# Kernel optimization log

Hardware: AMD Instinct MI355X
Metric: run time of the kernel (lower is better)

## Reference

```python
import jax, jax.numpy as jnp
import numpy as np

N = 200000      # nodes per graph batch side
E = 3200000     # edges per side (avg degree 16)
NG = 1000       # number of graphs per side
CIN = 64
F1, F2, F3, D = 64, 32, 16, 16
BN_EPS = 1e-5


def gin_conv(x, edge_index, eps, W1, b1, W2, b2, gamma, beta):
    # GINConv: nn((1+eps)*x + sum_{j->i} x_j), nn = Lin-ReLU-Lin-BatchNorm1d (batch stats)
    src, dst = edge_index[0], edge_index[1]
    agg = jax.ops.segment_sum(x[src], dst, num_segments=x.shape[0])
    h = (1.0 + eps) * x + agg
    h = jax.nn.relu(h @ W1 + b1) @ W2 + b2
    mu = jnp.mean(h, axis=0)
    var = jnp.var(h, axis=0)
    return gamma * (h - mu) * jax.lax.rsqrt(var + BN_EPS) + beta


def global_attention_readout(x, batch, W, b):
    # global_mean_pool -> sigmoid fc -> gated global_add_pool
    ones = jnp.ones((x.shape[0], 1), x.dtype)
    cnt = jax.ops.segment_sum(ones, batch, num_segments=NG)
    summ = jax.ops.segment_sum(x, batch, num_segments=NG)
    mean = summ / jnp.maximum(cnt, 1.0)
    c = jax.nn.sigmoid(mean @ W + b)          # [NG, F3]
    c_n = c[batch]                             # broadcast back to nodes
    gate = jax.nn.sigmoid(jnp.sum(x * c_n, axis=1, keepdims=True))
    return jax.ops.segment_sum(gate * x, batch, num_segments=NG)


def efn(h_i, h_j, aW1, ab1, aW2, ab2, mW, mb):
    h = jnp.concatenate([h_i, h_j], axis=1)   # [NG, 2*F3]
    att = jnp.tanh(jax.nn.relu(h @ aW1 + ab1) @ aW2 + ab2)
    enc = att * h + h
    return jax.nn.relu(enc @ mW + mb)         # [NG, D]


def setup_inputs() -> dict:
    key = jax.random.key(0)
    ks = iter(jax.random.split(key, 48))
    def nrm(shape, s=0.1):
        return jax.random.normal(next(ks), shape, jnp.float32) * s
    inp = {}
    inp["x_i"] = jax.random.normal(next(ks), (N, CIN), jnp.float32)
    inp["x_j"] = jax.random.normal(next(ks), (N, CIN), jnp.float32)
    inp["edge_index_i"] = jax.random.randint(next(ks), (2, E), 0, N, dtype=jnp.int32)
    inp["edge_index_j"] = jax.random.randint(next(ks), (2, E), 0, N, dtype=jnp.int32)
    inp["batch_i"] = jnp.sort(jax.random.randint(next(ks), (N,), 0, NG, dtype=jnp.int32))
    inp["batch_j"] = jnp.sort(jax.random.randint(next(ks), (N,), 0, NG, dtype=jnp.int32))
    # GINConv 1 (train_eps=True, init 0)
    inp["eps1"] = jnp.zeros((), jnp.float32)
    inp["g1_W1"], inp["g1_b1"] = nrm((CIN, F1)), jnp.zeros((F1,), jnp.float32)
    inp["g1_W2"], inp["g1_b2"] = nrm((F1, F1)), jnp.zeros((F1,), jnp.float32)
    inp["g1_g"], inp["g1_bt"] = jnp.ones((F1,), jnp.float32), jnp.zeros((F1,), jnp.float32)
    inp["eps2"] = jnp.zeros((), jnp.float32)
    inp["g2_W1"], inp["g2_b1"] = nrm((F1, F2)), jnp.zeros((F2,), jnp.float32)
    inp["g2_W2"], inp["g2_b2"] = nrm((F2, F2)), jnp.zeros((F2,), jnp.float32)
    inp["g2_g"], inp["g2_bt"] = jnp.ones((F2,), jnp.float32), jnp.zeros((F2,), jnp.float32)
    inp["eps3"] = jnp.zeros((), jnp.float32)
    inp["g3_W1"], inp["g3_b1"] = nrm((F2, F3)), jnp.zeros((F3,), jnp.float32)
    inp["g3_W2"], inp["g3_b2"] = nrm((F3, F3)), jnp.zeros((F3,), jnp.float32)
    inp["g3_g"], inp["g3_bt"] = jnp.ones((F3,), jnp.float32), jnp.zeros((F3,), jnp.float32)
    # global attention fc
    inp["att_W"], inp["att_b"] = nrm((F3, F3)), jnp.zeros((F3,), jnp.float32)
    # EFN: in=2*F3=32, reduction=4 -> 8
    inp["efn_aW1"], inp["efn_ab1"] = nrm((2 * F3, 8)), jnp.zeros((8,), jnp.float32)
    inp["efn_aW2"], inp["efn_ab2"] = nrm((8, 2 * F3)), jnp.zeros((2 * F3,), jnp.float32)
    inp["efn_mW"], inp["efn_mb"] = nrm((2 * F3, D)), jnp.zeros((D,), jnp.float32)
    # final fc: D -> D//2 -> 1
    inp["fc_W1"], inp["fc_b1"] = nrm((D, D // 2)), jnp.zeros((D // 2,), jnp.float32)
    inp["fc_W2"], inp["fc_b2"] = nrm((D // 2, 1)), jnp.zeros((1,), jnp.float32)
    return inp


def reference(x_i, x_j, edge_index_i, edge_index_j, batch_i, batch_j,
              eps1, g1_W1, g1_b1, g1_W2, g1_b2, g1_g, g1_bt,
              eps2, g2_W1, g2_b1, g2_W2, g2_b2, g2_g, g2_bt,
              eps3, g3_W1, g3_b1, g3_W2, g3_b2, g3_g, g3_bt,
              att_W, att_b,
              efn_aW1, efn_ab1, efn_aW2, efn_ab2, efn_mW, efn_mb,
              fc_W1, fc_b1, fc_W2, fc_b2):
    xi1 = gin_conv(x_i, edge_index_i, eps1, g1_W1, g1_b1, g1_W2, g1_b2, g1_g, g1_bt)
    xj1 = gin_conv(x_j, edge_index_j, eps1, g1_W1, g1_b1, g1_W2, g1_b2, g1_g, g1_bt)
    xi2 = gin_conv(xi1, edge_index_i, eps2, g2_W1, g2_b1, g2_W2, g2_b2, g2_g, g2_bt)
    xj2 = gin_conv(xj1, edge_index_j, eps2, g2_W1, g2_b1, g2_W2, g2_b2, g2_g, g2_bt)
    xi3 = gin_conv(xi2, edge_index_i, eps3, g3_W1, g3_b1, g3_W2, g3_b2, g3_g, g3_bt)
    xj3 = gin_conv(xj2, edge_index_j, eps3, g3_W1, g3_b1, g3_W2, g3_b2, g3_g, g3_bt)
    h_i = global_attention_readout(xi3, batch_i, att_W, att_b)
    h_j = global_attention_readout(xj3, batch_j, att_W, att_b)
    h_AB = efn(h_i, h_j, efn_aW1, efn_ab1, efn_aW2, efn_ab2, efn_mW, efn_mb)
    h_AA = efn(h_i, h_i, efn_aW1, efn_ab1, efn_aW2, efn_ab2, efn_mW, efn_mb)
    h_BB = efn(h_j, h_j, efn_aW1, efn_ab1, efn_aW2, efn_ab2, efn_mW, efn_mb)
    h_Ab = h_AB - h_BB
    h_aB = h_AB - h_AA
    score = (jax.nn.relu(h_AB @ fc_W1 + fc_b1) @ fc_W2 + fc_b2).squeeze(1)
    return (score, h_Ab, h_aB)
```

## Files before the change

kernel.cpp:

```cpp
#include <hip/hip_runtime.h>
#include <math.h>

#define NGRAPH 1000
#define NBK_MAX 400
#define PART_BLOCKS 256

typedef unsigned short ushort_t;
typedef __attribute__((ext_vector_type(8))) short short8;
typedef __attribute__((ext_vector_type(4))) float floatx4;

static __device__ inline ushort_t f2bf(float f) {
  unsigned u = __float_as_uint(f);
  u = (u + 0x7fffu + ((u >> 16) & 1u)) >> 16;
  return (ushort_t)u;
}


__global__ __launch_bounds__(1024) void bucket_hist(const int* __restrict__ dst, int E, int chunk,
                                                    int* __restrict__ hist, int nbk) {
  __shared__ int lh[NBK_MAX];
  for (int i = threadIdx.x; i < nbk; i += 1024) lh[i] = 0;
  __syncthreads();
  const int e0 = blockIdx.x * chunk;
  const int e1 = min(E, e0 + chunk);
  for (int e = e0 + threadIdx.x; e < e1; e += 1024) atomicAdd(&lh[dst[e] >> 9], 1);
  __syncthreads();
  int* row = hist + (size_t)blockIdx.x * nbk;
  for (int i = threadIdx.x; i < nbk; i += 1024) row[i] = lh[i];
}

__global__ __launch_bounds__(PART_BLOCKS) void colscan_par(int* __restrict__ hist, int nbk,
                                                           int* __restrict__ totals) {
  __shared__ int s[PART_BLOCKS];
  const int b = blockIdx.x;
  const int t = threadIdx.x;
  s[t] = hist[(size_t)t * nbk + b];
  __syncthreads();
  for (int off = 1; off < PART_BLOCKS; off <<= 1) {
    int u = (t >= off) ? s[t - off] : 0;
    __syncthreads();
    s[t] += u;
    __syncthreads();
  }
  const int exc = (t == 0) ? 0 : s[t - 1];
  hist[(size_t)t * nbk + b] = exc;
  if (t == PART_BLOCKS - 1) totals[b] = s[PART_BLOCKS - 1];
}

__global__ __launch_bounds__(1024) void scan_small(const int* __restrict__ in, int n,
                                                   int* __restrict__ out) {
  __shared__ int s[2048];
  const int t = threadIdx.x;
  s[t] = (t < n) ? in[t] : 0;
  s[t + 1024] = (t + 1024 < n) ? in[t + 1024] : 0;
  __syncthreads();
  for (int off = 1; off < 2048; off <<= 1) {
    int v0 = (t >= off) ? s[t - off] : 0;
    int v1 = ((t + 1024) >= off) ? s[t + 1024 - off] : 0;
    __syncthreads();
    s[t] += v0;
    s[t + 1024] += v1;
    __syncthreads();
  }
  if (t < n) out[t] = (t == 0) ? 0 : s[t - 1];
  const int u = t + 1024;
  if (u < n) out[u] = s[u - 1];
  if (t == 0) out[n] = s[n - 1];
}

__global__ __launch_bounds__(1024) void partition_kernel(const int* __restrict__ src,
                                                         const int* __restrict__ dst, int E,
                                                         int chunk, const int* __restrict__ hist,
                                                         const int* __restrict__ boff,
                                                         unsigned* __restrict__ ebuf, int nbk) {
  __shared__ int lbase[NBK_MAX];
  __shared__ int lcur[NBK_MAX];
  const int* row = hist + (size_t)blockIdx.x * nbk;
  for (int i = threadIdx.x; i < nbk; i += 1024) {
    lbase[i] = boff[i] + row[i];
    lcur[i] = 0;
  }
  __syncthreads();
  const int e0 = blockIdx.x * chunk;
  const int e1 = min(E, e0 + chunk);
  for (int e = e0 + threadIdx.x; e < e1; e += 1024) {
    int d = dst[e];
    int b = d >> 9;
    int pos = lbase[b] + atomicAdd(&lcur[b], 1);
    ebuf[pos] = ((unsigned)src[e] << 9) | (unsigned)(d & 511);
  }
}

__global__ __launch_bounds__(512) void bucket_csr(const unsigned* __restrict__ ebuf,
                                                  const int* __restrict__ boff,
                                                  int* __restrict__ row_ptr, int* __restrict__ col,
                                                  int N, int E) {
  __shared__ int cnt[512], cur[512];
  const int b = blockIdx.x;
  const int node0 = b << 9;
  const int nn = min(512, N - node0);
  const int es = boff[b], ee = boff[b + 1];
  const int t = threadIdx.x;
  cnt[t] = 0;
  __syncthreads();
  for (int e = es + t; e < ee; e += 512) atomicAdd(&cnt[ebuf[e] & 511u], 1);
  __syncthreads();
  for (int off = 1; off < 512; off <<= 1) {
    int v = (t >= off) ? cnt[t - off] : 0;
    __syncthreads();
    cnt[t] += v;
    __syncthreads();
  }
  int ex = (t == 0) ? 0 : cnt[t - 1];
  cur[t] = ex;
  if (t < nn) row_ptr[node0 + t] = es + ex;
  __syncthreads();
  for (int e = es + t; e < ee; e += 512) {
    unsigned u = ebuf[e];
    int li = (int)(u & 511u);
    int pos = es + atomicAdd(&cur[li], 1);
    col[pos] = (int)(u >> 9);
  }
  if (b == 0 && t == 0) row_ptr[N] = E;
}


template <int FIN, int FOUT, bool HAS_BN>
__global__ __launch_bounds__(256) void lin_mfma(const float* __restrict__ x,
                                                const float* __restrict__ W,
                                                const float* __restrict__ stats,
                                                const float* __restrict__ gamma,
                                                const float* __restrict__ beta, float invN,
                                                ushort_t* __restrict__ y, int n) {
  constexpr int KC = FIN / 32;
  constexpr int FT = FOUT / 16;
  __shared__ ushort_t Wbf[FIN * FOUT];
  __shared__ float scv[FIN], ofv[FIN];
  const int tid = threadIdx.x;
  for (int i = tid; i < FIN * FOUT; i += 256) Wbf[i] = f2bf(W[i]);
  for (int i = tid; i < FIN; i += 256) {
    if (HAS_BN) {
      float mu = stats[i] * invN;
      float var = stats[128 + i] * invN - mu * mu;
      float s = gamma[i] * rsqrtf(var + 1e-5f);
      scv[i] = s;
      ofv[i] = beta[i] - s * mu;
    } else {
      scv[i] = 1.f;
      ofv[i] = 0.f;
    }
  }
  __syncthreads();
  const int lane = tid & 63, wv = tid >> 6;
  const int colf = lane & 15, quad = lane >> 4, kbase = quad * 8;

  short8 Bf[FT][KC];
#pragma unroll
  for (int t = 0; t < FT; t++)
#pragma unroll
    for (int c = 0; c < KC; c++)
#pragma unroll
      for (int j = 0; j < 8; j++)
        Bf[t][c][j] = (short)Wbf[(c * 32 + kbase + j) * FOUT + t * 16 + colf];

  const floatx4 zero4 = {0.f, 0.f, 0.f, 0.f};
  const int ntiles = (n + 15) >> 4;
  for (int nt = blockIdx.x * 4 + wv; nt < ntiles; nt += gridDim.x * 4) {
    const int node0 = nt << 4;
    const int anode = node0 + colf;
    short8 Af[KC];
#pragma unroll
    for (int c = 0; c < KC; c++) {
      if (anode < n) {
        const int kk = c * 32 + kbase;
        const float* xp = x + (size_t)anode * FIN + kk;
        float4 xa = *(const float4*)xp;
        float4 xb = *(const float4*)(xp + 4);
        Af[c][0] = (short)f2bf(fmaf(xa.x, scv[kk + 0], ofv[kk + 0]));
        Af[c][1] = (short)f2bf(fmaf(xa.y, scv[kk + 1], ofv[kk + 1]));
        Af[c][2] = (short)f2bf(fmaf(xa.z, scv[kk + 2], ofv[kk + 2]));
        Af[c][3] = (short)f2bf(fmaf(xa.w, scv[kk + 3], ofv[kk + 3]));
        Af[c][4] = (short)f2bf(fmaf(xb.x, scv[kk + 4], ofv[kk + 4]));
        Af[c][5] = (short)f2bf(fmaf(xb.y, scv[kk + 5], ofv[kk + 5]));
        Af[c][6] = (short)f2bf(fmaf(xb.z, scv[kk + 6], ofv[kk + 6]));
        Af[c][7] = (short)f2bf(fmaf(xb.w, scv[kk + 7], ofv[kk + 7]));
      } else {
        Af[c] = short8{0, 0, 0, 0, 0, 0, 0, 0};
      }
    }
#pragma unroll
    for (int t = 0; t < FT; t++) {
      floatx4 acc = zero4;
#pragma unroll
      for (int c = 0; c < KC; c++)
        acc = __builtin_amdgcn_mfma_f32_16x16x32_bf16(Af[c], Bf[t][c], acc, 0, 0, 0);
#pragma unroll
      for (int r = 0; r < 4; r++) {
        const int row = node0 + quad * 4 + r;
        if (row < n) y[(size_t)row * FOUT + t * 16 + colf] = f2bf(acc[r]);
      }
    }
  }
}


template <int F>
__global__ __launch_bounds__(256) void lin2s_mfma(const ushort_t* __restrict__ m,
                                                  const float* __restrict__ W,
                                                  const float* __restrict__ b,
                                                  float* __restrict__ h,
                                                  float* __restrict__ stats, int n) {
  constexpr int KC = (F + 31) / 32;
  constexpr int FT = F / 16;
  __shared__ ushort_t Wbf[F * F];
  __shared__ float bs[F], ls[F], lsq[F];
  const int tid = threadIdx.x;
  for (int i = tid; i < F * F; i += 256) Wbf[i] = f2bf(W[i]);
  if (tid < F) {
    bs[tid] = b[tid];
    ls[tid] = 0.f;
    lsq[tid] = 0.f;
  }
  __syncthreads();
  const int lane = tid & 63, wv = tid >> 6;
  const int colf = lane & 15, quad = lane >> 4, kbase = quad * 8;

  short8 Bf[FT][KC];
#pragma unroll
  for (int t = 0; t < FT; t++)
#pragma unroll
    for (int c = 0; c < KC; c++)
#pragma unroll
      for (int j = 0; j < 8; j++) {
        const int k = c * 32 + kbase + j;
        Bf[t][c][j] = (k < F) ? (short)Wbf[k * F + t * 16 + colf] : (short)0;
      }

  const floatx4 zero4 = {0.f, 0.f, 0.f, 0.f};
  float ssum[FT], ssq[FT];
#pragma unroll
  for (int t = 0; t < FT; t++) {
    ssum[t] = 0.f;
    ssq[t] = 0.f;
  }

  const int ntiles = (n + 15) >> 4;
  for (int nt = blockIdx.x * 4 + wv; nt < ntiles; nt += gridDim.x * 4) {
    const int node0 = nt << 4;
    const int anode = node0 + colf;
    short8 Af[KC];
#pragma unroll
    for (int c = 0; c < KC; c++) {
      const int kk = c * 32 + kbase;
      if (anode < n && kk < F)
        Af[c] = *(const short8*)(m + (size_t)anode * F + kk);
      else
        Af[c] = short8{0, 0, 0, 0, 0, 0, 0, 0};
    }
#pragma unroll
    for (int t = 0; t < FT; t++) {
      floatx4 acc = zero4;
#pragma unroll
      for (int c = 0; c < KC; c++)
        acc = __builtin_amdgcn_mfma_f32_16x16x32_bf16(Af[c], Bf[t][c], acc, 0, 0, 0);
      const float bv = bs[t * 16 + colf];
#pragma unroll
      for (int r = 0; r < 4; r++) {
        const int row = node0 + quad * 4 + r;
        if (row < n) {
          float o = acc[r] + bv;
          h[(size_t)row * F + t * 16 + colf] = o;
          ssum[t] += o;
          ssq[t] += o * o;
        }
      }
    }
  }
#pragma unroll
  for (int t = 0; t < FT; t++) {
    atomicAdd(&ls[t * 16 + colf], ssum[t]);
    atomicAdd(&lsq[t * 16 + colf], ssq[t]);
  }
  __syncthreads();
  if (tid < F) {
    atomicAdd(&stats[tid], ls[tid]);
    atomicAdd(&stats[128 + tid], lsq[tid]);
  }
}


template <int F>
__global__ __launch_bounds__(256) void aggrelu_b(const ushort_t* __restrict__ y,
                                                 const int* __restrict__ row_ptr,
                                                 const int* __restrict__ col,
                                                 const float* __restrict__ epsp,
                                                 const float* __restrict__ b1,
                                                 ushort_t* __restrict__ m, int n) {
  constexpr int LPN = F / 8;
  constexpr int NPB = 256 / LPN;
  const int tid = threadIdx.x;
  const int ln = tid / LPN;
  const int fl = tid % LPN;
  const float e1 = 1.0f + epsp[0];
  const float4 b1a = ((const float4*)b1)[fl * 2];
  const float4 b1b = ((const float4*)b1)[fl * 2 + 1];

  const int node = blockIdx.x * NPB + ln;
  if (node >= n) return;
  const uint4* yr = (const uint4*)y;
  const size_t rowi = (size_t)node * LPN + fl;
  const int rs = row_ptr[node], re = row_ptr[node + 1];

  float acc[8];
#pragma unroll
  for (int j = 0; j < 8; j++) acc[j] = 0.f;

  auto addv = [&](uint4 v) {
    acc[0] += __uint_as_float(v.x << 16);
    acc[1] += __uint_as_float(v.x & 0xffff0000u);
    acc[2] += __uint_as_float(v.y << 16);
    acc[3] += __uint_as_float(v.y & 0xffff0000u);
    acc[4] += __uint_as_float(v.z << 16);
    acc[5] += __uint_as_float(v.z & 0xffff0000u);
    acc[6] += __uint_as_float(v.w << 16);
    acc[7] += __uint_as_float(v.w & 0xffff0000u);
  };

  int e = rs;
  for (; e + 8 <= re; e += 8) {
    int c0 = col[e], c1 = col[e + 1], c2 = col[e + 2], c3 = col[e + 3];
    int c4 = col[e + 4], c5 = col[e + 5], c6 = col[e + 6], c7 = col[e + 7];
    uint4 v0 = yr[(size_t)c0 * LPN + fl];
    uint4 v1 = yr[(size_t)c1 * LPN + fl];
    uint4 v2 = yr[(size_t)c2 * LPN + fl];
    uint4 v3 = yr[(size_t)c3 * LPN + fl];
    uint4 v4 = yr[(size_t)c4 * LPN + fl];
    uint4 v5 = yr[(size_t)c5 * LPN + fl];
    uint4 v6 = yr[(size_t)c6 * LPN + fl];
    uint4 v7 = yr[(size_t)c7 * LPN + fl];
    addv(v0);
    addv(v1);
    addv(v2);
    addv(v3);
    addv(v4);
    addv(v5);
    addv(v6);
    addv(v7);
  }
  for (; e + 4 <= re; e += 4) {
    int c0 = col[e], c1 = col[e + 1], c2 = col[e + 2], c3 = col[e + 3];
    uint4 v0 = yr[(size_t)c0 * LPN + fl];
    uint4 v1 = yr[(size_t)c1 * LPN + fl];
    uint4 v2 = yr[(size_t)c2 * LPN + fl];
    uint4 v3 = yr[(size_t)c3 * LPN + fl];
    addv(v0);
    addv(v1);
    addv(v2);
    addv(v3);
  }
  for (; e < re; e++) addv(yr[(size_t)col[e] * LPN + fl]);

  uint4 sv = yr[rowi];
  float r0, r1, r2, r3, r4, r5, r6, r7;
  r0 = fmaxf(fmaf(e1, __uint_as_float(sv.x << 16), acc[0]) + b1a.x, 0.f);
  r1 = fmaxf(fmaf(e1, __uint_as_float(sv.x & 0xffff0000u), acc[1]) + b1a.y, 0.f);
  r2 = fmaxf(fmaf(e1, __uint_as_float(sv.y << 16), acc[2]) + b1a.z, 0.f);
  r3 = fmaxf(fmaf(e1, __uint_as_float(sv.y & 0xffff0000u), acc[3]) + b1a.w, 0.f);
  r4 = fmaxf(fmaf(e1, __uint_as_float(sv.z << 16), acc[4]) + b1b.x, 0.f);
  r5 = fmaxf(fmaf(e1, __uint_as_float(sv.z & 0xffff0000u), acc[5]) + b1b.y, 0.f);
  r6 = fmaxf(fmaf(e1, __uint_as_float(sv.w << 16), acc[6]) + b1b.z, 0.f);
  r7 = fmaxf(fmaf(e1, __uint_as_float(sv.w & 0xffff0000u), acc[7]) + b1b.w, 0.f);
  uint4 o;
  o.x = (unsigned)f2bf(r0) | ((unsigned)f2bf(r1) << 16);
  o.y = (unsigned)f2bf(r2) | ((unsigned)f2bf(r3) << 16);
  o.z = (unsigned)f2bf(r4) | ((unsigned)f2bf(r5) << 16);
  o.w = (unsigned)f2bf(r6) | ((unsigned)f2bf(r7) << 16);
  ((uint4*)m)[rowi] = o;
}


__global__ __launch_bounds__(256) void readout_fused(
    const float* __restrict__ h3, const int* __restrict__ batch, int n,
    const float* __restrict__ stats, const float* __restrict__ gamma,
    const float* __restrict__ beta, float invN, const float* __restrict__ attW,
    const float* __restrict__ attb, float* __restrict__ hg, int ng) {
  __shared__ float sM[16], oM[16], red[16][17], meanM[16], cM[16];
  __shared__ int seg[2];
  const int tid = threadIdx.x;
  const int g = blockIdx.x;
  const int f = tid & 15, slot = tid >> 4;
  if (tid < 16) {
    float mu = stats[tid] * invN;
    float var = stats[128 + tid] * invN - mu * mu;
    float s = gamma[tid] * rsqrtf(var + 1e-5f);
    sM[tid] = s;
    oM[tid] = beta[tid] - s * mu;
  }
  if (tid >= 32 && tid < 34) {
    const int key = g + (tid - 32);
    int lo = 0, hi = n;
    while (lo < hi) {
      int mid = (lo + hi) >> 1;
      if (batch[mid] < key) lo = mid + 1; else hi = mid;
    }
    seg[tid - 32] = lo;
  }
  __syncthreads();
  const int s0 = seg[0], e0 = seg[1];
  const float sf = sM[f], of = oM[f];

  float acc = 0.f;
  for (int node = s0 + slot; node < e0; node += 16)
    acc += fmaf(h3[(size_t)node * 16 + f], sf, of);
  red[slot][f] = acc;
  __syncthreads();
  if (tid < 16) {
    float t = 0.f;
    for (int s = 0; s < 16; s++) t += red[s][tid];
    meanM[tid] = t / fmaxf((float)(e0 - s0), 1.f);
  }
  __syncthreads();
  if (tid < 16) {
    float a = attb[tid];
    for (int k = 0; k < 16; k++) a += meanM[k] * attW[k * 16 + tid];
    cM[tid] = 1.f / (1.f + expf(-a));
  }
  __syncthreads();
  const float cf = cM[f];
  float acc2 = 0.f;
  for (int node = s0 + slot; node < e0; node += 16) {
    float xv = fmaf(h3[(size_t)node * 16 + f], sf, of);
    float p = xv * cf;
    for (int m = 8; m >= 1; m >>= 1) p += __shfl_xor(p, m, 16);
    acc2 += xv / (1.f + expf(-p));
  }
  red[slot][f] = acc2;
  __syncthreads();
  if (tid < 16) {
    float t = 0.f;
    for (int s = 0; s < 16; s++) t += red[s][tid];
    hg[g * 16 + tid] = t;
  }
}


__global__ __launch_bounds__(256) void final3_kernel(
    const float* __restrict__ hgA, const float* __restrict__ hgB, const float* __restrict__ aW1,
    const float* __restrict__ ab1, const float* __restrict__ aW2, const float* __restrict__ ab2,
    const float* __restrict__ mW, const float* __restrict__ mb, const float* __restrict__ fcW1,
    const float* __restrict__ fcb1, const float* __restrict__ fcW2,
    const float* __restrict__ fcb2, float* __restrict__ out, int ng) {
  __shared__ float aW1s[256], aW2s[256], mWs[512], fcW1s[128];
  __shared__ float ab1s[8], ab2s[32], mbs[16], fcb1s[8], fcW2s[8];
  __shared__ float fcb2s;
  __shared__ float hb[16][33], m8b[16][9], encb[16][33], abb[16][17], tb[16][9];
  const int tid = threadIdx.x;
  aW1s[tid] = aW1[tid];
  aW2s[tid] = aW2[tid];
  mWs[tid] = mW[tid];
  mWs[256 + tid] = mW[256 + tid];
  if (tid < 128) fcW1s[tid] = fcW1[tid];
  if (tid < 8) {
    ab1s[tid] = ab1[tid];
    fcb1s[tid] = fcb1[tid];
    fcW2s[tid] = fcW2[tid];
  }
  if (tid < 32) ab2s[tid] = ab2[tid];
  if (tid < 16) mbs[tid] = mb[tid];
  if (tid == 0) fcb2s = fcb2[0];
  __syncthreads();

  const int g = tid >> 4;
  const int l = tid & 15;
  const int gg = blockIdx.x * 16 + g;
  const bool valid = gg < ng;
  const float hiv = valid ? hgA[gg * 16 + l] : 0.f;
  const float hjv = valid ? hgB[gg * 16 + l] : 0.f;
  float res[3];

#pragma unroll
  for (int p = 0; p < 3; p++) {
    float ha = (p == 2) ? hjv : hiv;
    float h2 = (p == 1) ? hiv : hjv;
    hb[g][l] = ha;
    hb[g][16 + l] = h2;
    __syncthreads();
    if (l < 8) {
      float t = ab1s[l];
#pragma unroll
      for (int k = 0; k < 32; k++) t += hb[g][k] * aW1s[k * 8 + l];
      m8b[g][l] = fmaxf(t, 0.f);
    }
    __syncthreads();
    float e0 = ab2s[l], e1 = ab2s[16 + l];
#pragma unroll
    for (int k = 0; k < 8; k++) {
      float mv = m8b[g][k];
      e0 += mv * aW2s[k * 32 + l];
      e1 += mv * aW2s[k * 32 + 16 + l];
    }
    float a0 = tanhf(e0), a1 = tanhf(e1);
    encb[g][l] = fmaf(a0, ha, ha);
    encb[g][16 + l] = fmaf(a1, h2, h2);
    __syncthreads();
    float o = mbs[l];
#pragma unroll
    for (int k = 0; k < 32; k++) o += encb[g][k] * mWs[k * 16 + l];
    res[p] = fmaxf(o, 0.f);
    __syncthreads();
  }

  if (valid) {
    out[ng + gg * 16 + l] = res[0] - res[2];
    out[ng + ng * 16 + gg * 16 + l] = res[0] - res[1];
  }
  abb[g][l] = res[0];
  __syncthreads();
  if (l < 8) {
    float t = fcb1s[l];
#pragma unroll
    for (int k = 0; k < 16; k++) t += abb[g][k] * fcW1s[k * 8 + l];
    tb[g][l] = fmaxf(t, 0.f);
  }
  __syncthreads();
  if (l == 0 && valid) {
    float sc = fcb2s;
#pragma unroll
    for (int o = 0; o < 8; o++) sc += tb[g][o] * fcW2s[o];
    out[gg] = sc;
  }
}


extern "C" void kernel_launch(void* const* d_in, const int* in_sizes, int n_in, void* d_out,
                              int out_size, void* d_ws, size_t ws_size, hipStream_t stream) {
  (void)n_in;
  (void)out_size;
  (void)ws_size;
  const int N = in_sizes[0] / 64;
  const int E = in_sizes[2] / 2;
  const int NG = NGRAPH;
  const int NBK = (N + 511) >> 9;
  const int CHUNK = (E + PART_BLOCKS - 1) / PART_BLOCKS;

  char* w = (char*)d_ws;
  auto alloc = [&](size_t bytes) -> void* {
    void* p = (void*)w;
    w += (bytes + 255) & ~(size_t)255;
    return p;
  };
  int* row_ptr = (int*)alloc((size_t)(N + 1) * 4);
  int* col = (int*)alloc((size_t)E * 4);
  int* hist = (int*)alloc((size_t)PART_BLOCKS * NBK * 4);
  int* totals = (int*)alloc((size_t)NBK * 4);
  int* boff = (int*)alloc((size_t)(NBK + 1) * 4);
  float* bufA = (float*)alloc((size_t)N * 64 * 4);
  float* bufB = (float*)alloc((size_t)N * 64 * 4);
  float* stats = (float*)alloc(3 * 256 * 4);
  float* hgA = (float*)alloc((size_t)NG * 16 * 4);
  float* hgB = (float*)alloc((size_t)NG * 16 * 4);

  unsigned* ebuf = (unsigned*)bufA;
  ushort_t* y1 = (ushort_t*)bufB;
  ushort_t* m1 = (ushort_t*)bufA;
  float* h1 = bufB;
  ushort_t* y2 = (ushort_t*)bufA;
  ushort_t* m2 = (ushort_t*)(bufA + (size_t)N * 16);
  float* h2 = bufB;
  ushort_t* y3 = (ushort_t*)bufA;
  ushort_t* m3 = (ushort_t*)(bufA + (size_t)N * 8);
  float* h3 = bufB;

  const float* attW = (const float*)d_in[27];
  const float* attb = (const float*)d_in[28];
  const float invN = 1.0f / (float)N;

  for (int s = 0; s < 2; s++) {
    const float* x0 = (const float*)d_in[s];
    const int* esrc = (const int*)d_in[2 + s];
    const int* edst = esrc + E;
    const int* batch = (const int*)d_in[4 + s];
    float* hg = s ? hgB : hgA;

    bucket_hist<<<PART_BLOCKS, 1024, 0, stream>>>(edst, E, CHUNK, hist, NBK);
    colscan_par<<<NBK, PART_BLOCKS, 0, stream>>>(hist, NBK, totals);
    scan_small<<<1, 1024, 0, stream>>>(totals, NBK, boff);
    partition_kernel<<<PART_BLOCKS, 1024, 0, stream>>>(esrc, edst, E, CHUNK, hist, boff, ebuf,
                                                       NBK);
    bucket_csr<<<NBK, 512, 0, stream>>>(ebuf, boff, row_ptr, col, N, E);

    hipMemsetAsync(stats, 0, 3 * 256 * 4, stream);

    lin_mfma<64, 64, false><<<512, 256, 0, stream>>>(
        x0, (const float*)d_in[7], nullptr, nullptr, nullptr, invN, y1, N);
    aggrelu_b<64><<<(N + 31) / 32, 256, 0, stream>>>(
        y1, row_ptr, col, (const float*)d_in[6], (const float*)d_in[8], m1, N);
    lin2s_mfma<64><<<512, 256, 0, stream>>>(m1, (const float*)d_in[9], (const float*)d_in[10],
                                            h1, stats, N);

    lin_mfma<64, 32, true><<<512, 256, 0, stream>>>(
        h1, (const float*)d_in[14], stats, (const float*)d_in[11], (const float*)d_in[12], invN,
        y2, N);
    aggrelu_b<32><<<(N + 63) / 64, 256, 0, stream>>>(
        y2, row_ptr, col, (const float*)d_in[13], (const float*)d_in[15], m2, N);
    lin2s_mfma<32><<<512, 256, 0, stream>>>(m2, (const float*)d_in[16], (const float*)d_in[17],
                                            h2, stats + 256, N);

    lin_mfma<32, 16, true><<<512, 256, 0, stream>>>(
        h2, (const float*)d_in[21], stats + 256, (const float*)d_in[18], (const float*)d_in[19],
        invN, y3, N);
    aggrelu_b<16><<<(N + 127) / 128, 256, 0, stream>>>(
        y3, row_ptr, col, (const float*)d_in[20], (const float*)d_in[22], m3, N);
    lin2s_mfma<16><<<512, 256, 0, stream>>>(m3, (const float*)d_in[23], (const float*)d_in[24],
                                            h3, stats + 512, N);

    readout_fused<<<NG, 256, 0, stream>>>(h3, batch, N, stats + 512, (const float*)d_in[25],
                                          (const float*)d_in[26], invN, attW, attb, hg, NG);
  }

  final3_kernel<<<(NG + 15) / 16, 256, 0, stream>>>(
      hgA, hgB, (const float*)d_in[29], (const float*)d_in[30], (const float*)d_in[31],
      (const float*)d_in[32], (const float*)d_in[33], (const float*)d_in[34],
      (const float*)d_in[35], (const float*)d_in[36], (const float*)d_in[37],
      (const float*)d_in[38], (float*)d_out, NG);
}
```

Baseline: 894.5 us.

## Store GIN hidden activations in fp16 and build both CSRs in batched launches

The lin2s outputs (h1, h2, h3) are now stored as fp16 instead of fp32, and the consuming lin_mfma and readout kernels read them as half. Those GEMMs also switch from bf16 to fp16 MFMA, with weights and inputs converted to _Float16. The bucket-sort CSR construction for both graph sides now runs as single 2D-grid launches instead of being repeated inside the per-side loop, so separate row_ptr/col buffers are kept per side. The aim is to halve activation memory traffic and give the CSR build kernels twice the blocks per launch. The cost is reduced precision and range on the intermediates, with a risk of fp16 overflow or accuracy loss.

```diff
diff --git a/kernel.cpp b/kernel.cpp
--- a/kernel.cpp
+++ b/kernel.cpp
@@ -7,6 +7,7 @@
 
 typedef unsigned short ushort_t;
 typedef __attribute__((ext_vector_type(8))) short short8;
+typedef __attribute__((ext_vector_type(8))) _Float16 half8;
 typedef __attribute__((ext_vector_type(4))) float floatx4;
 
 static __device__ inline ushort_t f2bf(float f) {
@@ -14,10 +15,19 @@
   u = (u + 0x7fffu + ((u >> 16) & 1u)) >> 16;
   return (ushort_t)u;
 }
-
-
-__global__ __launch_bounds__(1024) void bucket_hist(const int* __restrict__ dst, int E, int chunk,
-                                                    int* __restrict__ hist, int nbk) {
+static __device__ inline ushort_t f2h_bits(float f) {
+  return __builtin_bit_cast(ushort_t, (_Float16)f);
+}
+static __device__ inline float h2f_bits(ushort_t u) {
+  return (float)__builtin_bit_cast(_Float16, u);
+}
+
+
+__global__ __launch_bounds__(1024) void bucket_hist2(const int* __restrict__ dst0,
+                                                     const int* __restrict__ dst1, int E,
+                                                     int chunk, int* __restrict__ hist, int nbk) {
+  const int side = blockIdx.y;
+  const int* __restrict__ dst = side ? dst1 : dst0;
   __shared__ int lh[NBK_MAX];
   for (int i = threadIdx.x; i < nbk; i += 1024) lh[i] = 0;
   __syncthreads();
@@ -25,16 +35,19 @@
   const int e1 = min(E, e0 + chunk);
   for (int e = e0 + threadIdx.x; e < e1; e += 1024) atomicAdd(&lh[dst[e] >> 9], 1);
   __syncthreads();
-  int* row = hist + (size_t)blockIdx.x * nbk;
+  int* row = hist + ((size_t)side * PART_BLOCKS + blockIdx.x) * nbk;
   for (int i = threadIdx.x; i < nbk; i += 1024) row[i] = lh[i];
 }
 
-__global__ __launch_bounds__(PART_BLOCKS) void colscan_par(int* __restrict__ hist, int nbk,
-                                                           int* __restrict__ totals) {
+__global__ __launch_bounds__(PART_BLOCKS) void colscan_par2(int* __restrict__ hist, int nbk,
+                                                            int* __restrict__ totals) {
   __shared__ int s[PART_BLOCKS];
+  const int side = blockIdx.y;
+  int* __restrict__ hist_s = hist + (size_t)side * PART_BLOCKS * nbk;
+  int* __restrict__ totals_s = totals + side * nbk;
   const int b = blockIdx.x;
   const int t = threadIdx.x;
-  s[t] = hist[(size_t)t * nbk + b];
+  s[t] = hist_s[(size_t)t * nbk + b];
   __syncthreads();
   for (int off = 1; off < PART_BLOCKS; off <<= 1) {
     int u = (t >= off) ? s[t - off] : 0;
@@ -43,16 +56,19 @@
     __syncthreads();
   }
   const int exc = (t == 0) ? 0 : s[t - 1];
-  hist[(size_t)t * nbk + b] = exc;
-  if (t == PART_BLOCKS - 1) totals[b] = s[PART_BLOCKS - 1];
-}
-
-__global__ __launch_bounds__(1024) void scan_small(const int* __restrict__ in, int n,
-                                                   int* __restrict__ out) {
+  hist_s[(size_t)t * nbk + b] = exc;
+  if (t == PART_BLOCKS - 1) totals_s[b] = s[PART_BLOCKS - 1];
+}
+
+__global__ __launch_bounds__(1024) void scan_small2(const int* __restrict__ in, int n,
+                                                    int* __restrict__ out) {
   __shared__ int s[2048];
+  const int side = blockIdx.x;
+  const int* __restrict__ in_s = in + side * n;
+  int* __restrict__ out_s = out + side * (n + 1);
   const int t = threadIdx.x;
-  s[t] = (t < n) ? in[t] : 0;
-  s[t + 1024] = (t + 1024 < n) ? in[t + 1024] : 0;
+  s[t] = (t < n) ? in_s[t] : 0;
+  s[t + 1024] = (t + 1024 < n) ? in_s[t + 1024] : 0;
   __syncthreads();
   for (int off = 1; off < 2048; off <<= 1) {
     int v0 = (t >= off) ? s[t - off] : 0;
@@ -62,22 +78,30 @@
     s[t + 1024] += v1;
     __syncthreads();
   }
-  if (t < n) out[t] = (t == 0) ? 0 : s[t - 1];
+  if (t < n) out_s[t] = (t == 0) ? 0 : s[t - 1];
   const int u = t + 1024;
-  if (u < n) out[u] = s[u - 1];
-  if (t == 0) out[n] = s[n - 1];
-}
-
-__global__ __launch_bounds__(1024) void partition_kernel(const int* __restrict__ src,
-                                                         const int* __restrict__ dst, int E,
-                                                         int chunk, const int* __restrict__ hist,
-                                                         const int* __restrict__ boff,
-                                                         unsigned* __restrict__ ebuf, int nbk) {
+  if (u < n) out_s[u] = s[u - 1];
+  if (t == 0) out_s[n] = s[n - 1];
+}
+
+__global__ __launch_bounds__(1024) void partition2(const int* __restrict__ src0,
+                                                   const int* __restrict__ src1,
+                                                   const int* __restrict__ dst0,
+                                                   const int* __restrict__ dst1, int E, int chunk,
+                                                   const int* __restrict__ hist,
+                                                   const int* __restrict__ boff,
+                                                   unsigned* __restrict__ ebufA,
+                                                   unsigned* __restrict__ ebufB, int nbk) {
+  const int side = blockIdx.y;
+  const int* __restrict__ src = side ? src1 : src0;
+  const int* __restrict__ dst = side ? dst1 : dst0;
+  const int* __restrict__ boff_s = boff + side * (nbk + 1);
+  unsigned* __restrict__ ebuf = side ? ebufB : ebufA;
   __shared__ int lbase[NBK_MAX];
   __shared__ int lcur[NBK_MAX];
-  const int* row = hist + (size_t)blockIdx.x * nbk;
+  const int* row = hist + ((size_t)side * PART_BLOCKS + blockIdx.x) * nbk;
   for (int i = threadIdx.x; i < nbk; i += 1024) {
-    lbase[i] = boff[i] + row[i];
+    lbase[i] = boff_s[i] + row[i];
     lcur[i] = 0;
   }
   __syncthreads();
@@ -91,15 +115,24 @@
   }
 }
 
-__global__ __launch_bounds__(512) void bucket_csr(const unsigned* __restrict__ ebuf,
-                                                  const int* __restrict__ boff,
-                                                  int* __restrict__ row_ptr, int* __restrict__ col,
-                                                  int N, int E) {
+__global__ __launch_bounds__(512) void bucket_csr2(const unsigned* __restrict__ ebufA,
+                                                   const unsigned* __restrict__ ebufB,
+                                                   const int* __restrict__ boff,
+                                                   int* __restrict__ row_ptrA,
+                                                   int* __restrict__ colA,
+                                                   int* __restrict__ row_ptrB,
+                                                   int* __restrict__ colB, int N, int E,
+                                                   int nbk) {
   __shared__ int cnt[512], cur[512];
+  const int side = blockIdx.y;
+  const unsigned* __restrict__ ebuf = side ? ebufB : ebufA;
+  const int* __restrict__ boff_s = boff + side * (nbk + 1);
+  int* __restrict__ row_ptr = side ? row_ptrB : row_ptrA;
+  int* __restrict__ col = side ? colB : colA;
   const int b = blockIdx.x;
   const int node0 = b << 9;
   const int nn = min(512, N - node0);
-  const int es = boff[b], ee = boff[b + 1];
+  const int es = boff_s[b], ee = boff_s[b + 1];
   const int t = threadIdx.x;
   cnt[t] = 0;
   __syncthreads();
@@ -125,8 +158,8 @@
 }
 
 
-template <int FIN, int FOUT, bool HAS_BN>
-__global__ __launch_bounds__(256) void lin_mfma(const float* __restrict__ x,
+template <int FIN, int FOUT, bool HAS_BN, bool IN_HALF>
+__global__ __launch_bounds__(256) void lin_mfma(const void* __restrict__ xin,
                                                 const float* __restrict__ W,
                                                 const float* __restrict__ stats,
                                                 const float* __restrict__ gamma,
@@ -134,12 +167,12 @@
                                                 ushort_t* __restrict__ y, int n) {
   constexpr int KC = FIN / 32;
   constexpr int FT = FOUT / 16;
-  __shared__ ushort_t Wbf[FIN * FOUT];
+  __shared__ _Float16 Whf[FIN * FOUT];
   __shared__ float scv[FIN], ofv[FIN];
   const int tid = threadIdx.x;
-  for (int i = tid; i < FIN * FOUT; i += 256) Wbf[i] = f2bf(W[i]);
+  for (int i = tid; i < FIN * FOUT; i += 256) Whf[i] = (_Float16)W[i];
   for (int i = tid; i < FIN; i += 256) {
-    if (HAS_BN) {
+    if constexpr (HAS_BN) {
       float mu = stats[i] * invN;
       float var = stats[128 + i] * invN - mu * mu;
       float s = gamma[i] * rsqrtf(var + 1e-5f);
@@ -154,38 +187,46 @@
   const int lane = tid & 63, wv = tid >> 6;
   const int colf = lane & 15, quad = lane >> 4, kbase = quad * 8;
 
-  short8 Bf[FT][KC];
+  half8 Bf[FT][KC];
 #pragma unroll
   for (int t = 0; t < FT; t++)
 #pragma unroll
     for (int c = 0; c < KC; c++)
 #pragma unroll
       for (int j = 0; j < 8; j++)
-        Bf[t][c][j] = (short)Wbf[(c * 32 + kbase + j) * FOUT + t * 16 + colf];
+        Bf[t][c][j] = Whf[(c * 32 + kbase + j) * FOUT + t * 16 + colf];
 
   const floatx4 zero4 = {0.f, 0.f, 0.f, 0.f};
   const int ntiles = (n + 15) >> 4;
   for (int nt = blockIdx.x * 4 + wv; nt < ntiles; nt += gridDim.x * 4) {
     const int node0 = nt << 4;
     const int anode = node0 + colf;
-    short8 Af[KC];
+    half8 Af[KC];
 #pragma unroll
     for (int c = 0; c < KC; c++) {
       if (anode < n) {
         const int kk = c * 32 + kbase;
-        const float* xp = x + (size_t)anode * FIN + kk;
-        float4 xa = *(const float4*)xp;
-        float4 xb = *(const float4*)(xp + 4);
-        Af[c][0] = (short)f2bf(fmaf(xa.x, scv[kk + 0], ofv[kk + 0]));
-        Af[c][1] = (short)f2bf(fmaf(xa.y, scv[kk + 1], ofv[kk + 1]));
-        Af[c][2] = (short)f2bf(fmaf(xa.z, scv[kk + 2], ofv[kk + 2]));
-        Af[c][3] = (short)f2bf(fmaf(xa.w, scv[kk + 3], ofv[kk + 3]));
-        Af[c][4] = (short)f2bf(fmaf(xb.x, scv[kk + 4], ofv[kk + 4]));
-        Af[c][5] = (short)f2bf(fmaf(xb.y, scv[kk + 5], ofv[kk + 5]));
-        Af[c][6] = (short)f2bf(fmaf(xb.z, scv[kk + 6], ofv[kk + 6]));
-        Af[c][7] = (short)f2bf(fmaf(xb.w, scv[kk + 7], ofv[kk + 7]));
+        if constexpr (IN_HALF) {
+          const ushort_t* hp = (const ushort_t*)xin + (size_t)anode * FIN + kk;
+          half8 hv = *(const half8*)hp;
+#pragma unroll
+          for (int j = 0; j < 8; j++)
+            Af[c][j] = (_Float16)fmaf((float)hv[j], scv[kk + j], ofv[kk + j]);
+        } else {
+          const float* xp = (const float*)xin + (size_t)anode * FIN + kk;
+          float4 xa = *(const float4*)xp;
+          float4 xb = *(const float4*)(xp + 4);
+          Af[c][0] = (_Float16)fmaf(xa.x, scv[kk + 0], ofv[kk + 0]);
+          Af[c][1] = (_Float16)fmaf(xa.y, scv[kk + 1], ofv[kk + 1]);
+          Af[c][2] = (_Float16)fmaf(xa.z, scv[kk + 2], ofv[kk + 2]);
+          Af[c][3] = (_Float16)fmaf(xa.w, scv[kk + 3], ofv[kk + 3]);
+          Af[c][4] = (_Float16)fmaf(xb.x, scv[kk + 4], ofv[kk + 4]);
+          Af[c][5] = (_Float16)fmaf(xb.y, scv[kk + 5], ofv[kk + 5]);
+          Af[c][6] = (_Float16)fmaf(xb.z, scv[kk + 6], ofv[kk + 6]);
+          Af[c][7] = (_Float16)fmaf(xb.w, scv[kk + 7], ofv[kk + 7]);
+        }
       } else {
-        Af[c] = short8{0, 0, 0, 0, 0, 0, 0, 0};
+        Af[c] = half8{0, 0, 0, 0, 0, 0, 0, 0};
       }
     }
 #pragma unroll
@@ -193,7 +234,7 @@
       floatx4 acc = zero4;
 #pragma unroll
       for (int c = 0; c < KC; c++)
-        acc = __builtin_amdgcn_mfma_f32_16x16x32_bf16(Af[c], Bf[t][c], acc, 0, 0, 0);
+        acc = __builtin_amdgcn_mfma_f32_16x16x32_f16(Af[c], Bf[t][c], acc, 0, 0, 0);
 #pragma unroll
       for (int r = 0; r < 4; r++) {
         const int row = node0 + quad * 4 + r;
@@ -208,7 +249,7 @@
 __global__ __launch_bounds__(256) void lin2s_mfma(const ushort_t* __restrict__ m,
                                                   const float* __restrict__ W,
                                                   const float* __restrict__ b,
-                                                  float* __restrict__ h,
+                                                  ushort_t* __restrict__ h,
                                                   float* __restrict__ stats, int n) {
   constexpr int KC = (F + 31) / 32;
   constexpr int FT = F / 16;
@@ -269,7 +310,7 @@
         const int row = node0 + quad * 4 + r;
         if (row < n) {
           float o = acc[r] + bv;
-          h[(size_t)row * F + t * 16 + colf] = o;
+          h[(size_t)row * F + t * 16 + colf] = f2h_bits(o);
           ssum[t] += o;
           ssq[t] += o * o;
         }
@@ -380,7 +421,7 @@
 
 
 __global__ __launch_bounds__(256) void readout_fused(
-    const float* __restrict__ h3, const int* __restrict__ batch, int n,
+    const ushort_t* __restrict__ h3, const int* __restrict__ batch, int n,
     const float* __restrict__ stats, const float* __restrict__ gamma,
     const float* __restrict__ beta, float invN, const float* __restrict__ attW,
     const float* __restrict__ attb, float* __restrict__ hg, int ng) {
@@ -411,7 +452,7 @@
 
   float acc = 0.f;
   for (int node = s0 + slot; node < e0; node += 16)
-    acc += fmaf(h3[(size_t)node * 16 + f], sf, of);
+    acc += fmaf(h2f_bits(h3[(size_t)node * 16 + f]), sf, of);
   red[slot][f] = acc;
   __syncthreads();
   if (tid < 16) {
@@ -429,7 +470,7 @@
   const float cf = cM[f];
   float acc2 = 0.f;
   for (int node = s0 + slot; node < e0; node += 16) {
-    float xv = fmaf(h3[(size_t)node * 16 + f], sf, of);
+    float xv = fmaf(h2f_bits(h3[(size_t)node * 16 + f]), sf, of);
     float p = xv * cf;
     for (int m = 8; m >= 1; m >>= 1) p += __shfl_xor(p, m, 16);
     acc2 += xv / (1.f + expf(-p));
@@ -549,72 +590,80 @@
     w += (bytes + 255) & ~(size_t)255;
     return p;
   };
-  int* row_ptr = (int*)alloc((size_t)(N + 1) * 4);
-  int* col = (int*)alloc((size_t)E * 4);
-  int* hist = (int*)alloc((size_t)PART_BLOCKS * NBK * 4);
-  int* totals = (int*)alloc((size_t)NBK * 4);
-  int* boff = (int*)alloc((size_t)(NBK + 1) * 4);
-  float* bufA = (float*)alloc((size_t)N * 64 * 4);
-  float* bufB = (float*)alloc((size_t)N * 64 * 4);
-  float* stats = (float*)alloc(3 * 256 * 4);
+  int* row_ptrA = (int*)alloc((size_t)(N + 1) * 4);
+  int* colA = (int*)alloc((size_t)E * 4);
+  int* row_ptrB = (int*)alloc((size_t)(N + 1) * 4);
+  int* colB = (int*)alloc((size_t)E * 4);
+  int* hist = (int*)alloc((size_t)2 * PART_BLOCKS * NBK * 4);
+  int* totals = (int*)alloc((size_t)2 * NBK * 4);
+  int* boff = (int*)alloc((size_t)2 * (NBK + 1) * 4);
+  ushort_t* bufA = (ushort_t*)alloc((size_t)N * 64 * 2);
+  ushort_t* bufB = (ushort_t*)alloc((size_t)N * 64 * 2);
+  float* stats = (float*)alloc((size_t)2 * 768 * 4);
   float* hgA = (float*)alloc((size_t)NG * 16 * 4);
   float* hgB = (float*)alloc((size_t)NG * 16 * 4);
 
-  unsigned* ebuf = (unsigned*)bufA;
-  ushort_t* y1 = (ushort_t*)bufB;
-  ushort_t* m1 = (ushort_t*)bufA;
-  float* h1 = bufB;
-  ushort_t* y2 = (ushort_t*)bufA;
-  ushort_t* m2 = (ushort_t*)(bufA + (size_t)N * 16);
-  float* h2 = bufB;
-  ushort_t* y3 = (ushort_t*)bufA;
-  ushort_t* m3 = (ushort_t*)(bufA + (size_t)N * 8);
-  float* h3 = bufB;
-
+  unsigned* ebufA = (unsigned*)bufA;
+  unsigned* ebufB = ebufA + E;
+  ushort_t* y1 = bufB;
+  ushort_t* m1 = bufA;
+  ushort_t* h1 = bufB;
+  ushort_t* y2 = bufA;
+  ushort_t* m2 = bufA + (size_t)N * 32;
+  ushort_t* h2 = bufB;
+  ushort_t* y3 = bufA;
+  ushort_t* m3 = bufA + (size_t)N * 16;
+  ushort_t* h3 = bufB;
+
+  const int* esrc0 = (const int*)d_in[2];
+  const int* edst0 = esrc0 + E;
+  const int* esrc1 = (const int*)d_in[3];
+  const int* edst1 = esrc1 + E;
   const float* attW = (const float*)d_in[27];
   const float* attb = (const float*)d_in[28];
   const float invN = 1.0f / (float)N;
 
+  bucket_hist2<<<dim3(PART_BLOCKS, 2), 1024, 0, stream>>>(edst0, edst1, E, CHUNK, hist, NBK);
+  colscan_par2<<<dim3(NBK, 2), PART_BLOCKS, 0, stream>>>(hist, NBK, totals);
+  scan_small2<<<2, 1024, 0, stream>>>(totals, NBK, boff);
+  partition2<<<dim3(PART_BLOCKS, 2), 1024, 0, stream>>>(esrc0, esrc1, edst0, edst1, E, CHUNK,
+                                                        hist, boff, ebufA, ebufB, NBK);
+  bucket_csr2<<<dim3(NBK, 2), 512, 0, stream>>>(ebufA, ebufB, boff, row_ptrA, colA, row_ptrB,
+                                                colB, N, E, NBK);
+  hipMemsetAsync(stats, 0, 2 * 768 * 4, stream);
+
   for (int s = 0; s < 2; s++) {
     const float* x0 = (const float*)d_in[s];
-    const int* esrc = (const int*)d_in[2 + s];
-    const int* edst = esrc + E;
     const int* batch = (const int*)d_in[4 + s];
+    const int* row_ptr = s ? row_ptrB : row_ptrA;
+    const int* col = s ? colB : colA;
+    float* st = stats + s * 768;
     float* hg = s ? hgB : hgA;
 
-    bucket_hist<<<PART_BLOCKS, 1024, 0, stream>>>(edst, E, CHUNK, hist, NBK);
-    colscan_par<<<NBK, PART_BLOCKS, 0, stream>>>(hist, NBK, totals);
-    scan_small<<<1, 1024, 0, stream>>>(totals, NBK, boff);
-    partition_kernel<<<PART_BLOCKS, 1024, 0, stream>>>(esrc, edst, E, CHUNK, hist, boff, ebuf,
-                                                       NBK);
-    bucket_csr<<<NBK, 512, 0, stream>>>(ebuf, boff, row_ptr, col, N, E);
-
-    hipMemsetAsync(stats, 0, 3 * 256 * 4, stream);
-
-    lin_mfma<64, 64, false><<<512, 256, 0, stream>>>(
+    lin_mfma<64, 64, false, false><<<512, 256, 0, stream>>>(
         x0, (const float*)d_in[7], nullptr, nullptr, nullptr, invN, y1, N);
     aggrelu_b<64><<<(N + 31) / 32, 256, 0, stream>>>(
         y1, row_ptr, col, (const float*)d_in[6], (const float*)d_in[8], m1, N);
     lin2s_mfma<64><<<512, 256, 0, stream>>>(m1, (const float*)d_in[9], (const float*)d_in[10],
-                                            h1, stats, N);
-
-    lin_mfma<64, 32, true><<<512, 256, 0, stream>>>(
-        h1, (const float*)d_in[14], stats, (const float*)d_in[11], (const float*)d_in[12], invN,
+                                            h1, st, N);
+
+    lin_mfma<64, 32, true, true><<<512, 256, 0, stream>>>(
+        h1, (const float*)d_in[14], st, (const float*)d_in[11], (const float*)d_in[12], invN,
         y2, N);
     aggrelu_b<32><<<(N + 63) / 64, 256, 0, stream>>>(
         y2, row_ptr, col, (const float*)d_in[13], (const float*)d_in[15], m2, N);
     lin2s_mfma<32><<<512, 256, 0, stream>>>(m2, (const float*)d_in[16], (const float*)d_in[17],
-                                            h2, stats + 256, N);
-
-    lin_mfma<32, 16, true><<<512, 256, 0, stream>>>(
-        h2, (const float*)d_in[21], stats + 256, (const float*)d_in[18], (const float*)d_in[19],
+                                            h2, st + 256, N);
+
+    lin_mfma<32, 16, true, true><<<512, 256, 0, stream>>>(
+        h2, (const float*)d_in[21], st + 256, (const float*)d_in[18], (const float*)d_in[19],
         invN, y3, N);
     aggrelu_b<16><<<(N + 127) / 128, 256, 0, stream>>>(
         y3, row_ptr, col, (const float*)d_in[20], (const float*)d_in[22], m3, N);
     lin2s_mfma<16><<<512, 256, 0, stream>>>(m3, (const float*)d_in[23], (const float*)d_in[24],
-                                            h3, stats + 512, N);
-
-    readout_fused<<<NG, 256, 0, stream>>>(h3, batch, N, stats + 512, (const float*)d_in[25],
+                                            h3, st + 512, N);
+
+    readout_fused<<<NG, 256, 0, stream>>>(h3, batch, N, st + 512, (const float*)d_in[25],
                                           (const float*)d_in[26], invN, attW, attb, hg, NG);
   }
 
```

New measurement: 895.4 us. About the same (+0.1%).
